# Performance work log

Hardware: AMD Instinct MI355X
Metric: run time of the kernel (lower is better)

## Reference

```python
import jax, jax.numpy as jnp
import numpy as np

XYZ_MIN = -1.0
XYZ_MAX = 1.0
ALPHA_INIT = 1e-6
ACT_SHIFT = float(np.log(1.0 / (1.0 - ALPHA_INIT) - 1.0))  # density bias shift


def trilinear_sample(grid, xyz):
    """PyTorch F.grid_sample(mode='bilinear', align_corners=True) for 3D.
    grid: [C, D, H, W] (D<->z, H<->y, W<->x); xyz: [N,3] global coords in [XYZ_MIN, XYZ_MAX].
    Returns [N, C]."""
    C, D, H, W = grid.shape
    u = (xyz - XYZ_MIN) / (XYZ_MAX - XYZ_MIN)            # [N,3] in [0,1]
    sizes = jnp.array([W, H, D], dtype=xyz.dtype)
    pos = u * (sizes - 1.0)                               # align_corners=True mapping
    i0f = jnp.floor(pos)
    w1 = pos - i0f                                        # [N,3] frac weights
    w0 = 1.0 - w1
    maxi = jnp.array([W - 1, H - 1, D - 1], dtype=jnp.int32)
    i0 = jnp.clip(i0f.astype(jnp.int32), 0, maxi)
    i1 = jnp.minimum(i0 + 1, maxi)
    x0, y0, z0 = i0[:, 0], i0[:, 1], i0[:, 2]
    x1, y1, z1 = i1[:, 0], i1[:, 1], i1[:, 2]
    gf = grid.reshape(C, -1)                              # [C, D*H*W]

    def corner(z, y, x):
        lin = (z * H + y) * W + x                         # [N]
        return gf[:, lin]                                 # [C, N]

    wx0, wy0, wz0 = w0[:, 0], w0[:, 1], w0[:, 2]
    wx1, wy1, wz1 = w1[:, 0], w1[:, 1], w1[:, 2]
    out = (corner(z0, y0, x0) * (wz0 * wy0 * wx0)
           + corner(z0, y0, x1) * (wz0 * wy0 * wx1)
           + corner(z0, y1, x0) * (wz0 * wy1 * wx0)
           + corner(z0, y1, x1) * (wz0 * wy1 * wx1)
           + corner(z1, y0, x0) * (wz1 * wy0 * wx0)
           + corner(z1, y0, x1) * (wz1 * wy0 * wx1)
           + corner(z1, y1, x0) * (wz1 * wy1 * wx0)
           + corner(z1, y1, x1) * (wz1 * wy1 * wx1))
    return out.T                                          # [N, C]


def setup_inputs() -> dict:
    key = jax.random.key(0)
    k1, k2, k3, k4, k5 = jax.random.split(key, 5)
    R, P = 16384, 256
    # Keep all sampled points inside [-1, 1]^3 (in-bounds grid_sample).
    origins = (jax.random.uniform(k1, (R, 3), jnp.float32) - 0.5) * 0.5   # [-0.25, 0.25]
    d = jax.random.normal(k2, (R, 3), jnp.float32)
    directions = d / jnp.linalg.norm(d, axis=-1, keepdims=True) * 0.5     # norm 0.5
    lengths = jax.random.uniform(k3, (R, P), jnp.float32)                 # [0, 1)
    density_grid = jax.random.normal(k4, (1, 160, 160, 160), jnp.float32) * 0.1
    color_grid = jax.random.normal(k5, (3, 160, 160, 160), jnp.float32) * 0.1
    return {"origins": origins, "directions": directions, "lengths": lengths,
            "density_grid": density_grid, "color_grid": color_grid}


def reference(origins, directions, lengths, density_grid, color_grid):
    R, P = lengths.shape
    # ray_bundle_to_ray_points: origins + directions * lengths
    pts = origins[:, None, :] + directions[:, None, :] * lengths[:, :, None]  # [R,P,3]
    interval = jnp.linalg.norm(directions, axis=-1)[:, None, None]            # [R,1,1]
    flat = pts.reshape(-1, 3)
    raw_density = trilinear_sample(density_grid, flat).reshape(R, P, 1)
    # alpha = 1 - (1 + exp(density + shift)) ** (-interval)
    density = 1.0 - (1.0 + jnp.exp(raw_density + ACT_SHIFT)) ** (-interval)
    raw_color = trilinear_sample(color_grid, flat).reshape(R, P, 3)
    color = jax.nn.sigmoid(raw_color)
    return density, color
```

## Files before the change

### kernel.cpp

```cpp
#include <hip/hip_runtime.h>
#include <math.h>

#define NRAYS 16384
#define NPTS  256
#define GS    160
#define GS3   (GS*GS*GS)

#define ACT_SHIFT (-13.815509557963774f)
#define LOG2E     (1.4426950408889634f)

typedef float floatx2 __attribute__((ext_vector_type(2)));

__device__ __forceinline__ unsigned int pack4fp8(float d, float r, float g, float b) {
    int w = __builtin_amdgcn_cvt_pk_fp8_f32(d, r, 0, false);
    w     = __builtin_amdgcn_cvt_pk_fp8_f32(g, b, w, true);
    return (unsigned int)w;
}

__device__ __forceinline__ void acc2(unsigned int w, float cw,
                                     floatx2& sdr, floatx2& sgb) {
    floatx2 dr = __builtin_amdgcn_cvt_pk_f32_fp8((int)w, false);
    floatx2 gb = __builtin_amdgcn_cvt_pk_f32_fp8((int)w, true);
    floatx2 cw2 = {cw, cw};
    sdr += dr * cw2;
    sgb += gb * cw2;
}

__global__ __launch_bounds__(256)
void repack_fp8ypair_x4_kernel(const float* __restrict__ dgrid,
                               const float* __restrict__ cgrid,
                               uint4* __restrict__ out)
{
    const int c = blockIdx.x * 256 + threadIdx.x;
    const int i = c * 4;
    if (i >= GS3) return;
    const int y  = (i / GS) % GS;
    const int dy = (y < GS - 1) ? GS : 0;

    const float4 d0 = *reinterpret_cast<const float4*>(&dgrid[i]);
    const float4 r0 = *reinterpret_cast<const float4*>(&cgrid[i]);
    const float4 g0 = *reinterpret_cast<const float4*>(&cgrid[GS3 + i]);
    const float4 b0 = *reinterpret_cast<const float4*>(&cgrid[2*GS3 + i]);
    const float4 d1 = *reinterpret_cast<const float4*>(&dgrid[i + dy]);
    const float4 r1 = *reinterpret_cast<const float4*>(&cgrid[i + dy]);
    const float4 g1 = *reinterpret_cast<const float4*>(&cgrid[GS3 + i + dy]);
    const float4 b1 = *reinterpret_cast<const float4*>(&cgrid[2*GS3 + i + dy]);

    uint4 o0, o1;
    o0.x = pack4fp8(d0.x, r0.x, g0.x, b0.x);  o0.y = pack4fp8(d1.x, r1.x, g1.x, b1.x);
    o0.z = pack4fp8(d0.y, r0.y, g0.y, b0.y);  o0.w = pack4fp8(d1.y, r1.y, g1.y, b1.y);
    o1.x = pack4fp8(d0.z, r0.z, g0.z, b0.z);  o1.y = pack4fp8(d1.z, r1.z, g1.z, b1.z);
    o1.z = pack4fp8(d0.w, r0.w, g0.w, b0.w);  o1.w = pack4fp8(d1.w, r1.w, g1.w, b1.w);

    out[c*2 + 0] = o0;
    out[c*2 + 1] = o1;
}

__global__ __launch_bounds__(256)
void sample_fp8yp_kernel(const float* __restrict__ origins,
                         const float* __restrict__ directions,
                         const float* __restrict__ lengths,
                         const uint2* __restrict__ grid,
                         float* __restrict__ out_density,
                         float* __restrict__ out_color)
{
    const int r   = blockIdx.x;
    const int p   = threadIdx.x;
    const int idx = r * NPTS + p;

    const float t  = __builtin_nontemporal_load(&lengths[idx]);
    const float ox = origins[3*r+0], oy = origins[3*r+1], oz = origins[3*r+2];
    const float dx = directions[3*r+0], dy = directions[3*r+1], dz = directions[3*r+2];
    const float interval = sqrtf(dx*dx + dy*dy + dz*dz);

    const float half_sm1 = 0.5f * (float)(GS - 1);
    const float px = (ox + dx*t + 1.0f) * half_sm1;
    const float py = (oy + dy*t + 1.0f) * half_sm1;
    const float pz = (oz + dz*t + 1.0f) * half_sm1;

    const float fx = floorf(px), fy = floorf(py), fz = floorf(pz);

    int x0 = min(max((int)fx, 0), GS-2);
    int y0 = min(max((int)fy, 0), GS-2);
    int z0 = min(max((int)fz, 0), GS-2);

    const int i0 = (z0*GS + y0)*GS + x0;

    const uint4 ez0 = *reinterpret_cast<const uint4*>(&grid[i0]);
    const uint4 ez1 = *reinterpret_cast<const uint4*>(&grid[i0 + GS*GS]);

    const float wx1 = px - fx, wy1 = py - fy, wz1 = pz - fz;
    const float wx0 = 1.0f - wx1, wy0 = 1.0f - wy1, wz0 = 1.0f - wz1;
    const float c00 = wy0*wx0, c10 = wy1*wx0, c01 = wy0*wx1, c11 = wy1*wx1;

    floatx2 sdr = {0.f, 0.f}, sgb = {0.f, 0.f};
    acc2(ez0.x, wz0*c00, sdr, sgb);
    acc2(ez0.y, wz0*c10, sdr, sgb);
    acc2(ez0.z, wz0*c01, sdr, sgb);
    acc2(ez0.w, wz0*c11, sdr, sgb);
    acc2(ez1.x, wz1*c00, sdr, sgb);
    acc2(ez1.y, wz1*c10, sdr, sgb);
    acc2(ez1.z, wz1*c01, sdr, sgb);
    acc2(ez1.w, wz1*c11, sdr, sgb);

    const float a  = sdr.x + ACT_SHIFT;
    const float ea = __builtin_amdgcn_exp2f(LOG2E * a);
    const float L  = __builtin_amdgcn_logf(1.0f + ea);
    __builtin_nontemporal_store(1.0f - __builtin_amdgcn_exp2f(-interval * L),
                                &out_density[idx]);

    const float e1 = __builtin_amdgcn_exp2f(-LOG2E * sdr.y);
    const float e2 = __builtin_amdgcn_exp2f(-LOG2E * sgb.x);
    const float e3 = __builtin_amdgcn_exp2f(-LOG2E * sgb.y);
    float3 col;
    col.x = __builtin_amdgcn_rcpf(1.0f + e1);
    col.y = __builtin_amdgcn_rcpf(1.0f + e2);
    col.z = __builtin_amdgcn_rcpf(1.0f + e3);
    *reinterpret_cast<float3*>(&out_color[idx*3]) = col;
}

__device__ __forceinline__ float2 ld2(const float* p) {
    return *reinterpret_cast<const float2*>(p);
}

__global__ __launch_bounds__(256)
void dvgo_render_kernel(const float* __restrict__ origins,
                        const float* __restrict__ directions,
                        const float* __restrict__ lengths,
                        const float* __restrict__ dgrid,
                        const float* __restrict__ cgrid,
                        float* __restrict__ out_density,
                        float* __restrict__ out_color)
{
    const int r = blockIdx.x;
    const int p = threadIdx.x;
    const int idx = r * NPTS + p;

    const float t  = lengths[idx];
    const float ox = origins[3*r+0], oy = origins[3*r+1], oz = origins[3*r+2];
    const float dx = directions[3*r+0], dy = directions[3*r+1], dz = directions[3*r+2];
    const float interval = sqrtf(dx*dx + dy*dy + dz*dz);

    const float x = ox + dx*t;
    const float y = oy + dy*t;
    const float z = oz + dz*t;

    const float half_sm1 = 0.5f * (float)(GS - 1);
    const float px = (x + 1.0f) * half_sm1;
    const float py = (y + 1.0f) * half_sm1;
    const float pz = (z + 1.0f) * half_sm1;

    const float fx = floorf(px), fy = floorf(py), fz = floorf(pz);
    const float wx1 = px - fx, wy1 = py - fy, wz1 = pz - fz;
    const float wx0 = 1.0f - wx1, wy0 = 1.0f - wy1, wz0 = 1.0f - wz1;

    int x0 = (int)fx, y0 = (int)fy, z0 = (int)fz;
    x0 = min(max(x0, 0), GS-2);
    y0 = min(max(y0, 0), GS-2);
    z0 = min(max(z0, 0), GS-2);

    int rows[4];
    rows[0] = ((z0  )*GS + y0  )*GS + x0;
    rows[1] = ((z0  )*GS + y0+1)*GS + x0;
    rows[2] = ((z0+1)*GS + y0  )*GS + x0;
    rows[3] = ((z0+1)*GS + y0+1)*GS + x0;

    const float* bases[4] = {dgrid, cgrid, cgrid + GS3, cgrid + 2*GS3};

    float2 v[4][4];
    #pragma unroll
    for (int ch = 0; ch < 4; ++ch)
        #pragma unroll
        for (int rr = 0; rr < 4; ++rr)
            v[ch][rr] = ld2(bases[ch] + rows[rr]);

    float rw[4];
    rw[0] = wz0*wy0; rw[1] = wz0*wy1; rw[2] = wz1*wy0; rw[3] = wz1*wy1;

    float s[4];
    #pragma unroll
    for (int ch = 0; ch < 4; ++ch) {
        float acc = 0.0f;
        #pragma unroll
        for (int rr = 0; rr < 4; ++rr)
            acc = fmaf(rw[rr], fmaf(v[ch][rr].x, wx0, v[ch][rr].y * wx1), acc);
        s[ch] = acc;
    }

    const float a  = s[0] + ACT_SHIFT;
    const float sp = (a > 20.0f) ? a : log1pf(__expf(a));
    out_density[idx] = 1.0f - __expf(-interval * sp);

    #pragma unroll
    for (int c = 0; c < 3; ++c)
        out_color[idx*3 + c] = 1.0f / (1.0f + __expf(-s[c+1]));
}

extern "C" void kernel_launch(void* const* d_in, const int* in_sizes, int n_in,
                              void* d_out, int out_size, void* d_ws, size_t ws_size,
                              hipStream_t stream) {
    const float* origins    = (const float*)d_in[0];
    const float* directions = (const float*)d_in[1];
    const float* lengths    = (const float*)d_in[2];
    const float* dgrid      = (const float*)d_in[3];
    const float* cgrid      = (const float*)d_in[4];

    float* out_density = (float*)d_out;
    float* out_color   = (float*)d_out + NRAYS*NPTS;

    if (ws_size >= (size_t)GS3 * sizeof(uint2)) {
        uint2* ypairs = (uint2*)d_ws;
        repack_fp8ypair_x4_kernel<<<(GS3/4 + 255) / 256, 256, 0, stream>>>(
            dgrid, cgrid, (uint4*)ypairs);
        sample_fp8yp_kernel<<<NRAYS, NPTS, 0, stream>>>(
            origins, directions, lengths, ypairs, out_density, out_color);
    } else {
        dvgo_render_kernel<<<NRAYS, NPTS, 0, stream>>>(
            origins, directions, lengths, dgrid, cgrid, out_density, out_color);
    }
}
```

Baseline: 52.19 us.

## Process eight rays per block with double-buffered software-pipelined gathers

The sampling kernel now handles eight rays per 256-thread block instead of one. All eight lengths are loaded up front, and the two grid gathers for the next ray are issued before the current ray is decoded and activated, giving a two-stage software pipeline. The aim is more memory-level parallelism per thread and less per-block launch overhead, in exchange for higher register pressure and a grid 8x smaller, which could reduce occupancy or latency hiding.

```diff
diff --git a/kernel.cpp b/kernel.cpp
--- a/kernel.cpp
+++ b/kernel.cpp
@@ -4,6 +4,7 @@
 #define NRAYS 16384
 #define NPTS  256
 #define GS    160
+#define GS2   (GS*GS)
 #define GS3   (GS*GS*GS)
 
 #define ACT_SHIFT (-13.815509557963774f)
@@ -57,66 +58,86 @@
 }
 
 __global__ __launch_bounds__(256)
-void sample_fp8yp_kernel(const float* __restrict__ origins,
-                         const float* __restrict__ directions,
-                         const float* __restrict__ lengths,
-                         const uint2* __restrict__ grid,
-                         float* __restrict__ out_density,
-                         float* __restrict__ out_color)
+void sample_fp8yp_pipe_kernel(const float* __restrict__ origins,
+                              const float* __restrict__ directions,
+                              const float* __restrict__ lengths,
+                              const uint2* __restrict__ grid,
+                              float* __restrict__ out_density,
+                              float* __restrict__ out_color)
 {
-    const int r   = blockIdx.x;
-    const int p   = threadIdx.x;
-    const int idx = r * NPTS + p;
-
-    const float t  = __builtin_nontemporal_load(&lengths[idx]);
-    const float ox = origins[3*r+0], oy = origins[3*r+1], oz = origins[3*r+2];
-    const float dx = directions[3*r+0], dy = directions[3*r+1], dz = directions[3*r+2];
-    const float interval = sqrtf(dx*dx + dy*dy + dz*dz);
-
+    const int tid   = threadIdx.x;
+    const int r0    = blockIdx.x * 8;
+    const int base0 = r0 * NPTS + tid;
     const float half_sm1 = 0.5f * (float)(GS - 1);
-    const float px = (ox + dx*t + 1.0f) * half_sm1;
-    const float py = (oy + dy*t + 1.0f) * half_sm1;
-    const float pz = (oz + dz*t + 1.0f) * half_sm1;
-
-    const float fx = floorf(px), fy = floorf(py), fz = floorf(pz);
-
-    int x0 = min(max((int)fx, 0), GS-2);
-    int y0 = min(max((int)fy, 0), GS-2);
-    int z0 = min(max((int)fz, 0), GS-2);
-
-    const int i0 = (z0*GS + y0)*GS + x0;
-
-    const uint4 ez0 = *reinterpret_cast<const uint4*>(&grid[i0]);
-    const uint4 ez1 = *reinterpret_cast<const uint4*>(&grid[i0 + GS*GS]);
-
-    const float wx1 = px - fx, wy1 = py - fy, wz1 = pz - fz;
-    const float wx0 = 1.0f - wx1, wy0 = 1.0f - wy1, wz0 = 1.0f - wz1;
-    const float c00 = wy0*wx0, c10 = wy1*wx0, c01 = wy0*wx1, c11 = wy1*wx1;
-
-    floatx2 sdr = {0.f, 0.f}, sgb = {0.f, 0.f};
-    acc2(ez0.x, wz0*c00, sdr, sgb);
-    acc2(ez0.y, wz0*c10, sdr, sgb);
-    acc2(ez0.z, wz0*c01, sdr, sgb);
-    acc2(ez0.w, wz0*c11, sdr, sgb);
-    acc2(ez1.x, wz1*c00, sdr, sgb);
-    acc2(ez1.y, wz1*c10, sdr, sgb);
-    acc2(ez1.z, wz1*c01, sdr, sgb);
-    acc2(ez1.w, wz1*c11, sdr, sgb);
-
-    const float a  = sdr.x + ACT_SHIFT;
-    const float ea = __builtin_amdgcn_exp2f(LOG2E * a);
-    const float L  = __builtin_amdgcn_logf(1.0f + ea);
-    __builtin_nontemporal_store(1.0f - __builtin_amdgcn_exp2f(-interval * L),
-                                &out_density[idx]);
-
-    const float e1 = __builtin_amdgcn_exp2f(-LOG2E * sdr.y);
-    const float e2 = __builtin_amdgcn_exp2f(-LOG2E * sgb.x);
-    const float e3 = __builtin_amdgcn_exp2f(-LOG2E * sgb.y);
-    float3 col;
-    col.x = __builtin_amdgcn_rcpf(1.0f + e1);
-    col.y = __builtin_amdgcn_rcpf(1.0f + e2);
-    col.z = __builtin_amdgcn_rcpf(1.0f + e3);
-    *reinterpret_cast<float3*>(&out_color[idx*3]) = col;
+
+    float tv[8];
+    #pragma unroll
+    for (int i = 0; i < 8; ++i)
+        tv[i] = __builtin_nontemporal_load(&lengths[base0 + i*NPTS]);
+
+    uint4 e0[2], e1[2];
+    float cw[2][8];
+    float itv[2];
+
+#define ISSUE(s, i) {                                                        \
+    const int r = r0 + (i);                                                  \
+    const float ox = origins[3*r+0], oy = origins[3*r+1], oz = origins[3*r+2]; \
+    const float dx = directions[3*r+0], dy = directions[3*r+1], dz = directions[3*r+2]; \
+    itv[s] = sqrtf(dx*dx + dy*dy + dz*dz);                                   \
+    const float t  = tv[i];                                                  \
+    const float px = (ox + dx*t + 1.0f) * half_sm1;                          \
+    const float py = (oy + dy*t + 1.0f) * half_sm1;                          \
+    const float pz = (oz + dz*t + 1.0f) * half_sm1;                          \
+    const float fx = floorf(px), fy = floorf(py), fz = floorf(pz);           \
+    const int x0 = min(max((int)fx, 0), GS-2);                               \
+    const int y0 = min(max((int)fy, 0), GS-2);                               \
+    const int z0 = min(max((int)fz, 0), GS-2);                               \
+    const int i0 = (z0*GS + y0)*GS + x0;                                     \
+    e0[s] = *reinterpret_cast<const uint4*>(&grid[i0]);                      \
+    e1[s] = *reinterpret_cast<const uint4*>(&grid[i0 + GS2]);                \
+    const float wx1 = px - fx, wy1 = py - fy, wz1 = pz - fz;                 \
+    const float wx0 = 1.0f - wx1, wy0 = 1.0f - wy1, wz0 = 1.0f - wz1;        \
+    const float c00 = wy0*wx0, c10 = wy1*wx0, c01 = wy0*wx1, c11 = wy1*wx1;  \
+    cw[s][0] = wz0*c00; cw[s][1] = wz0*c10; cw[s][2] = wz0*c01; cw[s][3] = wz0*c11; \
+    cw[s][4] = wz1*c00; cw[s][5] = wz1*c10; cw[s][6] = wz1*c01; cw[s][7] = wz1*c11; \
+}
+
+#define FINISH(s, i) {                                                       \
+    floatx2 sdr = {0.f, 0.f}, sgb = {0.f, 0.f};                              \
+    acc2(e0[s].x, cw[s][0], sdr, sgb);                                       \
+    acc2(e0[s].y, cw[s][1], sdr, sgb);                                       \
+    acc2(e0[s].z, cw[s][2], sdr, sgb);                                       \
+    acc2(e0[s].w, cw[s][3], sdr, sgb);                                       \
+    acc2(e1[s].x, cw[s][4], sdr, sgb);                                       \
+    acc2(e1[s].y, cw[s][5], sdr, sgb);                                       \
+    acc2(e1[s].z, cw[s][6], sdr, sgb);                                       \
+    acc2(e1[s].w, cw[s][7], sdr, sgb);                                       \
+    const float a  = sdr.x + ACT_SHIFT;                                      \
+    const float ea = __builtin_amdgcn_exp2f(LOG2E * a);                      \
+    const float L  = __builtin_amdgcn_logf(1.0f + ea);                       \
+    const int  id  = base0 + (i)*NPTS;                                       \
+    __builtin_nontemporal_store(1.0f - __builtin_amdgcn_exp2f(-itv[s] * L),  \
+                                &out_density[id]);                           \
+    const float x1 = __builtin_amdgcn_exp2f(-LOG2E * sdr.y);                 \
+    const float x2 = __builtin_amdgcn_exp2f(-LOG2E * sgb.x);                 \
+    const float x3 = __builtin_amdgcn_exp2f(-LOG2E * sgb.y);                 \
+    float3 col;                                                              \
+    col.x = __builtin_amdgcn_rcpf(1.0f + x1);                                \
+    col.y = __builtin_amdgcn_rcpf(1.0f + x2);                                \
+    col.z = __builtin_amdgcn_rcpf(1.0f + x3);                                \
+    *reinterpret_cast<float3*>(&out_color[id*3]) = col;                      \
+}
+
+    ISSUE(0, 0);
+    #pragma unroll
+    for (int i = 0; i < 7; ++i) {
+        ISSUE((i+1)&1, i+1);
+        FINISH(i&1, i);
+    }
+    FINISH(1, 7);
+
+#undef ISSUE
+#undef FINISH
 }
 
 __device__ __forceinline__ float2 ld2(const float* p) {
@@ -212,7 +233,7 @@
         uint2* ypairs = (uint2*)d_ws;
         repack_fp8ypair_x4_kernel<<<(GS3/4 + 255) / 256, 256, 0, stream>>>(
             dgrid, cgrid, (uint4*)ypairs);
-        sample_fp8yp_kernel<<<NRAYS, NPTS, 0, stream>>>(
+        sample_fp8yp_pipe_kernel<<<NRAYS / 8, 256, 0, stream>>>(
             origins, directions, lengths, ypairs, out_density, out_color);
     } else {
         dvgo_render_kernel<<<NRAYS, NPTS, 0, stream>>>(
```

After: 53.27 us. 1.02x slower.
